# Kernel tuning notes

Hardware: AMD Instinct MI355X
Metric: run time of the kernel (lower is better)

Reference implementation:

```python
import jax, jax.numpy as jnp
import numpy as np

BLOCK_SIZE = 128
N_EMBD = 600
HEAD_SIZE = 75
BATCH = 512


def setup_inputs() -> dict:
    key = jax.random.key(0)
    kx, kq, kk, kv = jax.random.split(key, 4)
    x = jax.random.normal(kx, (BATCH, BLOCK_SIZE, N_EMBD), dtype=jnp.float32)
    # nn.Linear(n_embd, head_size, bias=False); store as [in, out] so y = x @ W
    s = 1.0 / np.sqrt(N_EMBD)
    Wq = jax.random.uniform(kq, (N_EMBD, HEAD_SIZE), jnp.float32, -s, s)
    Wk = jax.random.uniform(kk, (N_EMBD, HEAD_SIZE), jnp.float32, -s, s)
    Wv = jax.random.uniform(kv, (N_EMBD, HEAD_SIZE), jnp.float32, -s, s)
    return {"x": x, "Wq": Wq, "Wk": Wk, "Wv": Wv}


def reference(x, Wq, Wk, Wv):
    B, T, C = x.shape
    q = jnp.einsum("btc,ch->bth", x, Wq)
    k = jnp.einsum("btc,ch->bth", x, Wk)
    v = jnp.einsum("btc,ch->bth", x, Wv)
    # NOTE: source scales by C**-0.5 with C = n_embd (not head_size)
    scale = jnp.asarray(C, x.dtype) ** -0.5
    wei = jnp.einsum("bth,bsh->bts", q, k) * scale  # [B, T, T]
    causal = jnp.tril(jnp.ones((T, T), dtype=bool))
    wei = jnp.where(causal, wei, -jnp.inf)
    attn = jax.nn.softmax(wei, axis=-1)
    # dropout is identity in eval/reference mode
    return jnp.einsum("bts,bsh->bth", attn, v)
```

## Files before the change

kernel.cpp:

```cpp
#include <hip/hip_runtime.h>
#include <stdint.h>
#include <math.h>

#define TT 128
#define CC 600
#define HH 75

typedef __attribute__((ext_vector_type(8)))  short bh8;
typedef __attribute__((ext_vector_type(16))) float f32x16;
typedef __attribute__((ext_vector_type(4)))  float f32x4;

#define XA_OFF   0
#define WB_OFF   20480
#define P_OFF    0
#define PM_OFF   32768
#define PS_OFF   33792
#define Q_OFF    61440
#define K_OFF    94208
#define V_OFF    126976
#define LDS_BYTES 147456

__device__ __forceinline__ uint32_t f2bf1(float f) {
  uint32_t u = __float_as_uint(f);
  return (u + 0x7FFFu + ((u >> 16) & 1u)) >> 16;
}
__device__ __forceinline__ uint32_t packbf(float a, float b) {
  return f2bf1(a) | (f2bf1(b) << 16);
}
__device__ __forceinline__ float bfrt(float f) {
  return __uint_as_float(f2bf1(f) << 16);
}
__device__ __forceinline__ int swz(int row, int bytein) {
  return row * 256 + (bytein ^ ((row & 7) << 4));
}

__global__ void pack_w_kernel(const float* __restrict__ Wq, const float* __restrict__ Wk,
                              const float* __restrict__ Wv, uint16_t* __restrict__ wpack) {
  const int chunk = blockIdx.x;
  const int n     = threadIdx.x;
  const float* W = nullptr;
  int h = 0;
  if (n < 80)       { W = Wq; h = n; }
  else if (n < 160) { W = Wk; h = n - 80; }
  else if (n < 240) { W = Wv; h = n - 160; }
  const bool valid = (W != nullptr) && (h < 75);
  uint32_t u[20];
#pragma unroll
  for (int g = 0; g < 20; ++g) u[g] = 0u;
#pragma unroll
  for (int s = 0; s < 32; ++s) {
    const int k = chunk * 32 + s;
    float v = 0.f;
    if (valid && k < CC) v = W[k * HH + h];
    u[s >> 1] |= f2bf1(v) << ((s & 1) * 16);
  }
  uint32_t* dst = (uint32_t*)(wpack + (size_t)chunk * 10240 + (size_t)n * 40);
#pragma unroll
  for (int g = 0; g < 5; ++g)
    ((uint4*)dst)[g] = make_uint4(u[g*4], u[g*4+1], u[g*4+2], u[g*4+3]);
}

__global__ __launch_bounds__(512, 2) void head_kernel(
    const float* __restrict__ x, const uint16_t* __restrict__ wpack,
    float* __restrict__ out)
{
  __shared__ char smem[LDS_BYTES];
  const int tid  = threadIdx.x;
  const int b    = blockIdx.x;
  const int lane = tid & 63;
  const int wv   = tid >> 6;
  const int l31  = lane & 31;
  const int h5   = lane >> 5;

  const int m0 = (wv >> 2) * 64;
  const int n0 = (wv & 3) * 64;

  f32x16 acc[2][2];
#pragma unroll
  for (int mi = 0; mi < 2; ++mi)
#pragma unroll
    for (int ni = 0; ni < 2; ++ni)
#pragma unroll
      for (int r = 0; r < 16; ++r) acc[mi][ni][r] = 0.f;

  const int xt  = tid >> 2;
  const int xcg = tid & 3;
  const float* xrow = x + (size_t)b * (TT * CC) + (size_t)xt * CC;

  {
    float4 p0 = *(const float4*)(xrow + xcg * 4);
    float4 p1 = *(const float4*)(xrow + 16 + xcg * 4);
    const uint4* wc = (const uint4*)wpack;
    uint4 q0 = wc[tid];
    uint4 q1 = wc[tid + 512];
    uint4 q2 = make_uint4(0,0,0,0);
    if (tid < 256) q2 = wc[tid + 1024];
    char* xa = smem + XA_OFF;
    char* wb = smem + WB_OFF;
    *(uint2*)(xa + xt * 80 + xcg * 8)      = make_uint2(packbf(p0.x, p0.y), packbf(p0.z, p0.w));
    *(uint2*)(xa + xt * 80 + 32 + xcg * 8) = make_uint2(packbf(p1.x, p1.y), packbf(p1.z, p1.w));
    *(uint4*)(wb + tid * 16)          = q0;
    *(uint4*)(wb + (tid + 512) * 16)  = q1;
    if (tid < 256) *(uint4*)(wb + (tid + 1024) * 16) = q2;
    __syncthreads();
  }

  for (int c = 0; c < 19; ++c) {
    const int  buf  = c & 1;
    const bool more = (c + 1 < 19);
    float4 p0, p1; uint4 q0, q1, q2;
    if (more) {
      const int cc = c + 1;
      p0 = *(const float4*)(xrow + cc * 32 + xcg * 4);
      const int c2 = cc * 32 + 16 + xcg * 4;
      p1 = *(const float4*)(xrow + ((c2 < CC) ? c2 : 0));
      const uint4* wc = (const uint4*)(wpack + (size_t)cc * 10240);
      q0 = wc[tid];
      q1 = wc[tid + 512];
      if (tid < 256) q2 = wc[tid + 1024];
    }
    const char* xa = smem + XA_OFF + buf * 10240;
    const char* wb = smem + WB_OFF + buf * 20480;
#pragma unroll
    for (int ks = 0; ks < 2; ++ks) {
      bh8 af[2], bf[2];
#pragma unroll
      for (int mi = 0; mi < 2; ++mi)
        af[mi] = *(const bh8*)(xa + (m0 + mi * 32 + l31) * 80 + ks * 32 + h5 * 16);
#pragma unroll
      for (int ni = 0; ni < 2; ++ni)
        bf[ni] = *(const bh8*)(wb + (n0 + ni * 32 + l31) * 80 + ks * 32 + h5 * 16);
#pragma unroll
      for (int mi = 0; mi < 2; ++mi)
#pragma unroll
        for (int ni = 0; ni < 2; ++ni)
          acc[mi][ni] = __builtin_amdgcn_mfma_f32_32x32x16_bf16(af[mi], bf[ni], acc[mi][ni], 0, 0, 0);
    }
    if (more) {
      const int nb = buf ^ 1;
      char* xaw = smem + XA_OFF + nb * 10240;
      char* wbw = smem + WB_OFF + nb * 20480;
      *(uint2*)(xaw + xt * 80 + xcg * 8)      = make_uint2(packbf(p0.x, p0.y), packbf(p0.z, p0.w));
      *(uint2*)(xaw + xt * 80 + 32 + xcg * 8) = make_uint2(packbf(p1.x, p1.y), packbf(p1.z, p1.w));
      *(uint4*)(wbw + tid * 16)          = q0;
      *(uint4*)(wbw + (tid + 512) * 16)  = q1;
      if (tid < 256) *(uint4*)(wbw + (tid + 1024) * 16) = q2;
    }
    __syncthreads();
  }

#pragma unroll
  for (int mi = 0; mi < 2; ++mi) {
    const int tb = m0 + mi * 32;
#pragma unroll
    for (int ni = 0; ni < 2; ++ni) {
      const int nn = n0 + ni * 32 + l31;
      if (n0 + ni * 32 < 160) {
        char* base  = smem + (nn < 80 ? Q_OFF : K_OFF);
        const int hb = (nn < 80 ? nn : nn - 80) * 2;
#pragma unroll
        for (int r = 0; r < 16; ++r) {
          const int t = tb + (r & 3) + 8 * (r >> 2) + 4 * h5;
          *(uint16_t*)(base + swz(t, hb)) = (uint16_t)f2bf1(acc[mi][ni][r]);
        }
      } else if (nn < 240) {
        const int hh2 = nn - 160;
#pragma unroll
        for (int g = 0; g < 4; ++g) {
          const int t0 = tb + 8 * g + 4 * h5;
          *(uint2*)(smem + V_OFF + swz(hh2, t0 * 2)) =
            make_uint2(packbf(acc[mi][ni][4*g],   acc[mi][ni][4*g+1]),
                       packbf(acc[mi][ni][4*g+2], acc[mi][ni][4*g+3]));
        }
      }
    }
  }
  __syncthreads();

  const int mt2 = wv & 1;
  const int tq  = (wv >> 1) * 32 + l31;
  f32x16 sac[2];
#pragma unroll
  for (int ts2 = 0; ts2 < 2; ++ts2)
#pragma unroll
    for (int r = 0; r < 16; ++r) sac[ts2][r] = 0.f;

#pragma unroll
  for (int ks = 0; ks < 5; ++ks) {
    const int kb = ks * 32 + h5 * 16;
    const bh8 qf = *(const bh8*)(smem + Q_OFF + swz(tq, kb));
#pragma unroll
    for (int ts2 = 0; ts2 < 2; ++ts2) {
      const int sr = (mt2 * 2 + ts2) * 32 + l31;
      const bh8 kf = *(const bh8*)(smem + K_OFF + swz(sr, kb));
      sac[ts2] = __builtin_amdgcn_mfma_f32_32x32x16_bf16(kf, qf, sac[ts2], 0, 0, 0);
    }
  }

  float pvv[32];
  float vmax = -INFINITY;
  const float scl = 0.040824829046386302f;
#pragma unroll
  for (int ts2 = 0; ts2 < 2; ++ts2) {
    const int st = (mt2 * 2 + ts2) * 32;
#pragma unroll
    for (int r = 0; r < 16; ++r) {
      const int s = st + (r & 3) + 8 * (r >> 2) + 4 * h5;
      float v = sac[ts2][r] * scl;
      v = (s <= tq) ? v : -INFINITY;
      pvv[ts2 * 16 + r] = v;
      vmax = fmaxf(vmax, v);
    }
  }
  vmax = fmaxf(vmax, __shfl_xor(vmax, 32));
  float* pmb = (float*)(smem + PM_OFF);
  float* psb = (float*)(smem + PS_OFF);
  if (h5 == 0) pmb[mt2 * 128 + tq] = vmax;
  __syncthreads();
  const float mrow = fmaxf(pmb[tq], pmb[128 + tq]);
  float sum = 0.f;
#pragma unroll
  for (int i = 0; i < 32; ++i) {
    const float p = bfrt(__expf(pvv[i] - mrow));
    pvv[i] = p;
    sum += p;
  }
  sum += __shfl_xor(sum, 32);
  if (h5 == 0) psb[mt2 * 128 + tq] = sum;
#pragma unroll
  for (int ts2 = 0; ts2 < 2; ++ts2) {
    const int st = (mt2 * 2 + ts2) * 32;
#pragma unroll
    for (int g = 0; g < 4; ++g) {
      const int s0 = st + 8 * g + 4 * h5;
      *(uint2*)(smem + P_OFF + swz(tq, s0 * 2)) =
        make_uint2(packbf(pvv[ts2*16+4*g],   pvv[ts2*16+4*g+1]),
                   packbf(pvv[ts2*16+4*g+2], pvv[ts2*16+4*g+3]));
    }
  }
  __syncthreads();

  const int l15   = lane & 15;
  const int q4    = lane >> 4;
  const int trow0 = wv * 16;
  f32x4 oac[5];
#pragma unroll
  for (int nt = 0; nt < 5; ++nt)
#pragma unroll
    for (int r = 0; r < 4; ++r) oac[nt][r] = 0.f;

#pragma unroll
  for (int ks = 0; ks < 4; ++ks) {
    const int kb = ks * 64 + q4 * 16;
    const bh8 pf = *(const bh8*)(smem + P_OFF + swz(trow0 + l15, kb));
#pragma unroll
    for (int nt = 0; nt < 5; ++nt) {
      const bh8 vf = *(const bh8*)(smem + V_OFF + swz(nt * 16 + l15, kb));
      oac[nt] = __builtin_amdgcn_mfma_f32_16x16x32_bf16(pf, vf, oac[nt], 0, 0, 0);
    }
  }

  const float* psf = (const float*)(smem + PS_OFF);
  float rinv[4];
#pragma unroll
  for (int r = 0; r < 4; ++r) {
    const int t = trow0 + q4 * 4 + r;
    rinv[r] = 1.0f / (psf[t] + psf[128 + t]);
  }
  float* ob = out + (size_t)b * (TT * HH);
#pragma unroll
  for (int nt = 0; nt < 5; ++nt) {
    const int h = nt * 16 + l15;
    if (h < 75) {
#pragma unroll
      for (int r = 0; r < 4; ++r) {
        const int t = trow0 + q4 * 4 + r;
        ob[t * HH + h] = oac[nt][r] * rinv[r];
      }
    }
  }
}

extern "C" void kernel_launch(void* const* d_in, const int* in_sizes, int n_in,
                              void* d_out, int out_size, void* d_ws, size_t ws_size,
                              hipStream_t stream) {
  (void)in_sizes; (void)n_in; (void)out_size; (void)ws_size;
  const float* x  = (const float*)d_in[0];
  const float* Wq = (const float*)d_in[1];
  const float* Wk = (const float*)d_in[2];
  const float* Wv = (const float*)d_in[3];
  uint16_t* wpack = (uint16_t*)d_ws;
  float* out = (float*)d_out;
  pack_w_kernel<<<19, 256, 0, stream>>>(Wq, Wk, Wv, wpack);
  head_kernel<<<512, 512, 0, stream>>>(x, wpack, out);
}
```

Before: 260.8 us.

## Load W fragments directly from global and shrink LDS to raise occupancy

Weights are repacked into an MFMA-fragment-ready layout so each wave loads its B operands straight from global/L2 into registers, removing the W double buffer from LDS. The Q/K layout is reorganised into 16-wide head slabs, and the P matrix is written in two halves that reuse a smaller buffer, with extra barriers. Together this cuts LDS from 144KB to 80KB, and launch bounds move to 4 blocks per CU, aiming to overlap more blocks. The trade-off is repeated global weight reads per wave each chunk and more synchronisation in the PV stage.

```diff
diff --git a/kernel.cpp b/kernel.cpp
--- a/kernel.cpp
+++ b/kernel.cpp
@@ -10,15 +10,14 @@
 typedef __attribute__((ext_vector_type(16))) float f32x16;
 typedef __attribute__((ext_vector_type(4)))  float f32x4;
 
-#define XA_OFF   0
-#define WB_OFF   20480
-#define P_OFF    0
-#define PM_OFF   32768
-#define PS_OFF   33792
-#define Q_OFF    61440
-#define K_OFF    94208
-#define V_OFF    126976
-#define LDS_BYTES 147456
+#define XA_OFF 0
+#define P_OFF  0
+#define PM_OFF 16384
+#define PS_OFF 17408
+#define Q_OFF  20480
+#define K_OFF  40960
+#define V_OFF  61440
+#define LDS_BYTES 81920
 
 __device__ __forceinline__ uint32_t f2bf1(float f) {
   uint32_t u = __float_as_uint(f);
@@ -33,34 +32,34 @@
 __device__ __forceinline__ int swz(int row, int bytein) {
   return row * 256 + (bytein ^ ((row & 7) << 4));
 }
+__device__ __forceinline__ int pswz(int row, int bytein) {
+  return row * 128 + (bytein ^ ((row & 7) << 4));
+}
 
 __global__ void pack_w_kernel(const float* __restrict__ Wq, const float* __restrict__ Wk,
                               const float* __restrict__ Wv, uint16_t* __restrict__ wpack) {
-  const int chunk = blockIdx.x;
-  const int n     = threadIdx.x;
-  const float* W = nullptr;
-  int h = 0;
-  if (n < 80)       { W = Wq; h = n; }
-  else if (n < 160) { W = Wk; h = n - 80; }
-  else if (n < 240) { W = Wv; h = n - 160; }
-  const bool valid = (W != nullptr) && (h < 75);
-  uint32_t u[20];
-#pragma unroll
-  for (int g = 0; g < 20; ++g) u[g] = 0u;
-#pragma unroll
-  for (int s = 0; s < 32; ++s) {
-    const int k = chunk * 32 + s;
-    float v = 0.f;
-    if (valid && k < CC) v = W[k * HH + h];
-    u[s >> 1] |= f2bf1(v) << ((s & 1) * 16);
-  }
-  uint32_t* dst = (uint32_t*)(wpack + (size_t)chunk * 10240 + (size_t)n * 40);
-#pragma unroll
-  for (int g = 0; g < 5; ++g)
-    ((uint4*)dst)[g] = make_uint4(u[g*4], u[g*4+1], u[g*4+2], u[g*4+3]);
-}
-
-__global__ __launch_bounds__(512, 2) void head_kernel(
+  const int cs  = blockIdx.x;
+  const int tid = threadIdx.x;
+  const int n   = tid >> 1;
+  const int h5  = tid & 1;
+  const int sec = n / 80;
+  const int h   = n - sec * 80;
+  const float* W = (sec == 0) ? Wq : (sec == 1) ? Wk : (sec == 2) ? Wv : nullptr;
+  const bool valid = (W != nullptr) && (h < HH);
+  const int k0 = cs * 16 + h5 * 8;
+  uint32_t u[4] = {0u, 0u, 0u, 0u};
+  if (valid) {
+#pragma unroll
+    for (int j = 0; j < 8; ++j) {
+      const int k = k0 + j;
+      float v = (k < CC) ? W[k * HH + h] : 0.f;
+      u[j >> 1] |= f2bf1(v) << ((j & 1) * 16);
+    }
+  }
+  ((uint4*)wpack)[cs * 512 + n * 2 + h5] = make_uint4(u[0], u[1], u[2], u[3]);
+}
+
+__global__ __launch_bounds__(512, 4) void head_kernel(
     const float* __restrict__ x, const uint16_t* __restrict__ wpack,
     float* __restrict__ out)
 {
@@ -86,65 +85,52 @@
   const int xt  = tid >> 2;
   const int xcg = tid & 3;
   const float* xrow = x + (size_t)b * (TT * CC) + (size_t)xt * CC;
+  const bh8* wfp = (const bh8*)wpack;
+  const int woff = (n0 + l31) * 2 + h5;
 
   {
     float4 p0 = *(const float4*)(xrow + xcg * 4);
     float4 p1 = *(const float4*)(xrow + 16 + xcg * 4);
-    const uint4* wc = (const uint4*)wpack;
-    uint4 q0 = wc[tid];
-    uint4 q1 = wc[tid + 512];
-    uint4 q2 = make_uint4(0,0,0,0);
-    if (tid < 256) q2 = wc[tid + 1024];
     char* xa = smem + XA_OFF;
-    char* wb = smem + WB_OFF;
     *(uint2*)(xa + xt * 80 + xcg * 8)      = make_uint2(packbf(p0.x, p0.y), packbf(p0.z, p0.w));
     *(uint2*)(xa + xt * 80 + 32 + xcg * 8) = make_uint2(packbf(p1.x, p1.y), packbf(p1.z, p1.w));
-    *(uint4*)(wb + tid * 16)          = q0;
-    *(uint4*)(wb + (tid + 512) * 16)  = q1;
-    if (tid < 256) *(uint4*)(wb + (tid + 1024) * 16) = q2;
     __syncthreads();
   }
 
   for (int c = 0; c < 19; ++c) {
     const int  buf  = c & 1;
     const bool more = (c + 1 < 19);
-    float4 p0, p1; uint4 q0, q1, q2;
+    bh8 w00 = wfp[(c * 2 + 0) * 512 + 0  + woff];
+    bh8 w01 = wfp[(c * 2 + 0) * 512 + 64 + woff];
+    bh8 w10 = wfp[(c * 2 + 1) * 512 + 0  + woff];
+    bh8 w11 = wfp[(c * 2 + 1) * 512 + 64 + woff];
+    float4 p0, p1;
     if (more) {
       const int cc = c + 1;
       p0 = *(const float4*)(xrow + cc * 32 + xcg * 4);
       const int c2 = cc * 32 + 16 + xcg * 4;
       p1 = *(const float4*)(xrow + ((c2 < CC) ? c2 : 0));
-      const uint4* wc = (const uint4*)(wpack + (size_t)cc * 10240);
-      q0 = wc[tid];
-      q1 = wc[tid + 512];
-      if (tid < 256) q2 = wc[tid + 1024];
     }
     const char* xa = smem + XA_OFF + buf * 10240;
-    const char* wb = smem + WB_OFF + buf * 20480;
 #pragma unroll
     for (int ks = 0; ks < 2; ++ks) {
-      bh8 af[2], bf[2];
+      bh8 af[2];
 #pragma unroll
       for (int mi = 0; mi < 2; ++mi)
         af[mi] = *(const bh8*)(xa + (m0 + mi * 32 + l31) * 80 + ks * 32 + h5 * 16);
-#pragma unroll
-      for (int ni = 0; ni < 2; ++ni)
-        bf[ni] = *(const bh8*)(wb + (n0 + ni * 32 + l31) * 80 + ks * 32 + h5 * 16);
-#pragma unroll
-      for (int mi = 0; mi < 2; ++mi)
-#pragma unroll
-        for (int ni = 0; ni < 2; ++ni)
-          acc[mi][ni] = __builtin_amdgcn_mfma_f32_32x32x16_bf16(af[mi], bf[ni], acc[mi][ni], 0, 0, 0);
+      const bh8 b0 = ks ? w10 : w00;
+      const bh8 b1 = ks ? w11 : w01;
+#pragma unroll
+      for (int mi = 0; mi < 2; ++mi) {
+        acc[mi][0] = __builtin_amdgcn_mfma_f32_32x32x16_bf16(af[mi], b0, acc[mi][0], 0, 0, 0);
+        acc[mi][1] = __builtin_amdgcn_mfma_f32_32x32x16_bf16(af[mi], b1, acc[mi][1], 0, 0, 0);
+      }
     }
     if (more) {
       const int nb = buf ^ 1;
       char* xaw = smem + XA_OFF + nb * 10240;
-      char* wbw = smem + WB_OFF + nb * 20480;
       *(uint2*)(xaw + xt * 80 + xcg * 8)      = make_uint2(packbf(p0.x, p0.y), packbf(p0.z, p0.w));
       *(uint2*)(xaw + xt * 80 + 32 + xcg * 8) = make_uint2(packbf(p1.x, p1.y), packbf(p1.z, p1.w));
-      *(uint4*)(wbw + tid * 16)          = q0;
-      *(uint4*)(wbw + (tid + 512) * 16)  = q1;
-      if (tid < 256) *(uint4*)(wbw + (tid + 1024) * 16) = q2;
     }
     __syncthreads();
   }
@@ -155,13 +141,13 @@
 #pragma unroll
     for (int ni = 0; ni < 2; ++ni) {
       const int nn = n0 + ni * 32 + l31;
-      if (n0 + ni * 32 < 160) {
-        char* base  = smem + (nn < 80 ? Q_OFF : K_OFF);
-        const int hb = (nn < 80 ? nn : nn - 80) * 2;
+      if (nn < 160) {
+        const int h = (nn < 80) ? nn : nn - 80;
+        char* base = smem + ((nn < 80) ? Q_OFF : K_OFF) + (h >> 4) * 4096 + (h & 15) * 2;
 #pragma unroll
         for (int r = 0; r < 16; ++r) {
           const int t = tb + (r & 3) + 8 * (r >> 2) + 4 * h5;
-          *(uint16_t*)(base + swz(t, hb)) = (uint16_t)f2bf1(acc[mi][ni][r]);
+          *(uint16_t*)(base + t * 32) = (uint16_t)f2bf1(acc[mi][ni][r]);
         }
       } else if (nn < 240) {
         const int hh2 = nn - 160;
@@ -187,12 +173,11 @@
 
 #pragma unroll
   for (int ks = 0; ks < 5; ++ks) {
-    const int kb = ks * 32 + h5 * 16;
-    const bh8 qf = *(const bh8*)(smem + Q_OFF + swz(tq, kb));
+    const bh8 qf = *(const bh8*)(smem + Q_OFF + ks * 4096 + tq * 32 + h5 * 16);
 #pragma unroll
     for (int ts2 = 0; ts2 < 2; ++ts2) {
       const int sr = (mt2 * 2 + ts2) * 32 + l31;
-      const bh8 kf = *(const bh8*)(smem + K_OFF + swz(sr, kb));
+      const bh8 kf = *(const bh8*)(smem + K_OFF + ks * 4096 + sr * 32 + h5 * 16);
       sac[ts2] = __builtin_amdgcn_mfma_f32_32x32x16_bf16(kf, qf, sac[ts2], 0, 0, 0);
     }
   }
@@ -227,15 +212,16 @@
   }
   sum += __shfl_xor(sum, 32);
   if (h5 == 0) psb[mt2 * 128 + tq] = sum;
-#pragma unroll
-  for (int ts2 = 0; ts2 < 2; ++ts2) {
-    const int st = (mt2 * 2 + ts2) * 32;
-#pragma unroll
-    for (int g = 0; g < 4; ++g) {
-      const int s0 = st + 8 * g + 4 * h5;
-      *(uint2*)(smem + P_OFF + swz(tq, s0 * 2)) =
-        make_uint2(packbf(pvv[ts2*16+4*g],   pvv[ts2*16+4*g+1]),
-                   packbf(pvv[ts2*16+4*g+2], pvv[ts2*16+4*g+3]));
+  if (mt2 == 0) {
+#pragma unroll
+    for (int ts2 = 0; ts2 < 2; ++ts2) {
+#pragma unroll
+      for (int g = 0; g < 4; ++g) {
+        const int sl = ts2 * 32 + 8 * g + 4 * h5;
+        *(uint2*)(smem + P_OFF + pswz(tq, sl * 2)) =
+          make_uint2(packbf(pvv[ts2*16+4*g],   pvv[ts2*16+4*g+1]),
+                     packbf(pvv[ts2*16+4*g+2], pvv[ts2*16+4*g+3]));
+      }
     }
   }
   __syncthreads();
@@ -250,15 +236,39 @@
     for (int r = 0; r < 4; ++r) oac[nt][r] = 0.f;
 
 #pragma unroll
-  for (int ks = 0; ks < 4; ++ks) {
-    const int kb = ks * 64 + q4 * 16;
-    const bh8 pf = *(const bh8*)(smem + P_OFF + swz(trow0 + l15, kb));
+  for (int ksl = 0; ksl < 2; ++ksl) {
+    const int kb = ksl * 64 + q4 * 16;
+    const bh8 pf = *(const bh8*)(smem + P_OFF + pswz(trow0 + l15, kb));
 #pragma unroll
     for (int nt = 0; nt < 5; ++nt) {
       const bh8 vf = *(const bh8*)(smem + V_OFF + swz(nt * 16 + l15, kb));
       oac[nt] = __builtin_amdgcn_mfma_f32_16x16x32_bf16(pf, vf, oac[nt], 0, 0, 0);
     }
   }
+  __syncthreads();
+  if (mt2 == 1) {
+#pragma unroll
+    for (int ts2 = 0; ts2 < 2; ++ts2) {
+#pragma unroll
+      for (int g = 0; g < 4; ++g) {
+        const int sl = ts2 * 32 + 8 * g + 4 * h5;
+        *(uint2*)(smem + P_OFF + pswz(tq, sl * 2)) =
+          make_uint2(packbf(pvv[ts2*16+4*g],   pvv[ts2*16+4*g+1]),
+                     packbf(pvv[ts2*16+4*g+2], pvv[ts2*16+4*g+3]));
+      }
+    }
+  }
+  __syncthreads();
+#pragma unroll
+  for (int ksl = 0; ksl < 2; ++ksl) {
+    const int kb = ksl * 64 + q4 * 16;
+    const bh8 pf = *(const bh8*)(smem + P_OFF + pswz(trow0 + l15, kb));
+#pragma unroll
+    for (int nt = 0; nt < 5; ++nt) {
+      const bh8 vf = *(const bh8*)(smem + V_OFF + swz(nt * 16 + l15, 128 + kb));
+      oac[nt] = __builtin_amdgcn_mfma_f32_16x16x32_bf16(pf, vf, oac[nt], 0, 0, 0);
+    }
+  }
 
   const float* psf = (const float*)(smem + PS_OFF);
   float rinv[4];
@@ -271,7 +281,7 @@
 #pragma unroll
   for (int nt = 0; nt < 5; ++nt) {
     const int h = nt * 16 + l15;
-    if (h < 75) {
+    if (h < HH) {
 #pragma unroll
       for (int r = 0; r < 4; ++r) {
         const int t = trow0 + q4 * 4 + r;
@@ -291,6 +301,6 @@
   const float* Wv = (const float*)d_in[3];
   uint16_t* wpack = (uint16_t*)d_ws;
   float* out = (float*)d_out;
-  pack_w_kernel<<<19, 256, 0, stream>>>(Wq, Wk, Wv, wpack);
+  pack_w_kernel<<<38, 512, 0, stream>>>(Wq, Wk, Wv, wpack);
   head_kernel<<<512, 512, 0, stream>>>(x, wpack, out);
 }
```

Measured after the change: 249.8 us. 4.3% less time.
